# Optimization experiments

Measured on AMD Instinct MI355X. Metric: run time of the kernel, lower is better.

## Reference

```python
import jax, jax.numpy as jnp
import numpy as np

N_USERS, N_ITEMS, D, L = 100000, 30000, 64, 2
N = N_USERS + N_ITEMS
NNZ_ADJ, NNZ_SYM, NNZ_HERB = 4000000, 1600000, 480000


def spmm(rows, cols, vals, x, n):
    # sparse [n, m] @ dense [m, d] via gather + segment_sum
    return jax.ops.segment_sum(vals[:, None] * x[cols], rows, num_segments=n)


def setup_inputs():
    key = jax.random.key(0)
    ks = jax.random.split(key, 19)
    s = np.float32(1.0 / np.sqrt(D))  # xavier-like scale, keeps tanh unsaturated
    return {
        'user_embedding': jax.random.normal(ks[0], (N_USERS, D), jnp.float32) * s,
        'item_embedding': jax.random.normal(ks[1], (N_ITEMS, D), jnp.float32) * s,
        'adj_vals': jax.random.uniform(ks[2], (NNZ_ADJ,), jnp.float32),
        'sym_vals': jax.random.uniform(ks[3], (NNZ_SYM,), jnp.float32),
        'herb_vals': jax.random.uniform(ks[4], (NNZ_HERB,), jnp.float32),
        'Q_user': jax.random.normal(ks[5], (L, D, D), jnp.float32) * s,
        'Q_item': jax.random.normal(ks[6], (L, D, D), jnp.float32) * s,
        'W_gc_user': jax.random.normal(ks[7], (L, 2 * D, D), jnp.float32) * s,
        'W_gc_item': jax.random.normal(ks[8], (L, 2 * D, D), jnp.float32) * s,
        'b_gc_user': jax.random.normal(ks[9], (L, D), jnp.float32) * s,
        'b_gc_item': jax.random.normal(ks[10], (L, D), jnp.float32) * s,
        'M_user': jax.random.normal(ks[11], (D, D), jnp.float32) * s,
        'M_item': jax.random.normal(ks[12], (D, D), jnp.float32) * s,
        'adj_rows': jax.random.randint(ks[13], (NNZ_ADJ,), 0, N, jnp.int32),
        'adj_cols': jax.random.randint(ks[14], (NNZ_ADJ,), 0, N, jnp.int32),
        'sym_rows': jax.random.randint(ks[15], (NNZ_SYM,), 0, N_USERS, jnp.int32),
        'sym_cols': jax.random.randint(ks[16], (NNZ_SYM,), 0, N_USERS, jnp.int32),
        'herb_rows': jax.random.randint(ks[17], (NNZ_HERB,), 0, N_ITEMS, jnp.int32),
        'herb_cols': jax.random.randint(ks[18], (NNZ_HERB,), 0, N_ITEMS, jnp.int32),
    }


def reference(user_embedding, item_embedding, adj_vals, sym_vals, herb_vals,
              Q_user, Q_item, W_gc_user, W_gc_item, b_gc_user, b_gc_item,
              M_user, M_item, adj_rows, adj_cols, sym_rows, sym_cols,
              herb_rows, herb_cols):
    ego0 = jnp.concatenate([user_embedding, item_embedding], axis=0)  # [N, D]

    def graphsage_branch(Q, W, b):
        ego = ego0
        for k in range(L):  # loop over fixed small n_layers
            agg = spmm(adj_rows, adj_cols, adj_vals, ego, N)           # neighbor aggregate
            h = jnp.tanh(agg @ Q[k])                                    # Q transform
            ego = jnp.tanh(jnp.concatenate([ego, h], axis=1) @ W[k] + b[k])
            # mess_dropout = 0 -> identity (eval mode)
        nrm = jnp.sqrt(jnp.sum(ego * ego, axis=1, keepdims=True))
        return ego / jnp.maximum(nrm, 1e-12)                            # F.normalize(p=2, dim=1)

    u_all = graphsage_branch(Q_user, W_gc_user, b_gc_user)
    i_all = graphsage_branch(Q_item, W_gc_item, b_gc_item)
    u_g = u_all[:N_USERS]
    i_g = i_all[N_USERS:]

    user_pair = jnp.tanh(spmm(sym_rows, sym_cols, sym_vals, user_embedding, N_USERS) @ M_user)
    item_pair = jnp.tanh(spmm(herb_rows, herb_cols, herb_vals, item_embedding, N_ITEMS) @ M_item)

    # fusion == 'add'
    return jnp.concatenate([u_g + user_pair, i_g + item_pair], axis=0)  # [N, D]
```

## Files before the change

kernel.cpp:

```cpp
#include <hip/hip_runtime.h>
#include <hip/hip_fp16.h>

#define NU 100000
#define NI 30000
#define NT 130000
#define D  64
#define NNZ_ADJ  4000000
#define NNZ_SYM  1600000
#define NNZ_HERB 480000

#define CHUNK 4096
#define BROWS 512

#define NBLK_ADJ  977
#define NBLK_SYM  391
#define NBLK_HERB 118

#define NBUCK_ADJ  254
#define NBUCK_SYM  196
#define NBUCK_HERB 59
#define CAP_ADJ  17000
#define CAP_SYM  9500
#define CAP_HERB 9500

#define OFF_QU0 0
#define OFF_QI0 4096
#define OFF_QU1 8192
#define OFF_QI1 12288
#define OFF_WU0 16384
#define OFF_WI0 24576
#define OFF_WU1 32768
#define OFF_WI1 40960
#define OFF_MU  49152
#define OFF_MI  53248
#define WT_ELEMS 57344

typedef _Float16 f16x8 __attribute__((ext_vector_type(8)));
typedef float f32x4 __attribute__((ext_vector_type(4)));

__device__ inline f32x4 mfma_16x16x32(f16x8 a, f16x8 b, f32x4 c) {
  return __builtin_amdgcn_mfma_f32_16x16x32_f16(a, b, c, 0, 0, 0);
}
__device__ inline f16x8 ld8h(const __half* p) { return *(const f16x8*)p; }

__device__ inline float pk_val(unsigned p) {
  return __half2float(__ushort_as_half((unsigned short)(p & 0x7fffu)));
}

__global__ __launch_bounds__(256) void binA_all(
    const int* __restrict__ r0, const int* __restrict__ c0,
    const float* __restrict__ v0, uint2* __restrict__ st0, int* __restrict__ bc0,
    const int* __restrict__ r1, const int* __restrict__ c1,
    const float* __restrict__ v1, uint2* __restrict__ st1, int* __restrict__ bc1,
    const int* __restrict__ r2, const int* __restrict__ c2,
    const float* __restrict__ v2, uint2* __restrict__ st2, int* __restrict__ bc2) {
  __shared__ int cnt[256], lexc[256], cur[256], gbase[256], wt[4];
  __shared__ uint2 lpk[CHUNK];
  __shared__ unsigned char bid[CHUNK];
  int blk = blockIdx.x;
  const int* rows; const int* cols; const float* vals;
  uint2* staging; int* bcnt; int nnz, cap, base;
  if (blk < NBLK_ADJ) {
    rows = r0; cols = c0; vals = v0; staging = st0; bcnt = bc0;
    nnz = NNZ_ADJ; cap = CAP_ADJ; base = blk * CHUNK;
  } else if (blk < NBLK_ADJ + NBLK_SYM) {
    rows = r1; cols = c1; vals = v1; staging = st1; bcnt = bc1;
    nnz = NNZ_SYM; cap = CAP_SYM; base = (blk - NBLK_ADJ) * CHUNK;
  } else {
    rows = r2; cols = c2; vals = v2; staging = st2; bcnt = bc2;
    nnz = NNZ_HERB; cap = CAP_HERB; base = (blk - NBLK_ADJ - NBLK_SYM) * CHUNK;
  }
  int tid = threadIdx.x;
  int lim = min(CHUNK, nnz - base);
  cnt[tid] = 0;
  __syncthreads();
  for (int j = tid; j < lim; j += 256) {
    int r = rows[base + j];
    atomicAdd(&cnt[r >> 9], 1);
  }
  __syncthreads();
  int lane = tid & 63, w = tid >> 6;
  int v = cnt[tid];
  int s = v;
#pragma unroll
  for (int o = 1; o < 64; o <<= 1) {
    int t = __shfl_up(s, o, 64);
    if (lane >= o) s += t;
  }
  if (lane == 63) wt[w] = s;
  __syncthreads();
  int woff = 0;
  for (int j = 0; j < w; ++j) woff += wt[j];
  int exc = woff + s - v;
  lexc[tid] = exc;
  cur[tid] = exc;
  gbase[tid] = (v > 0) ? atomicAdd(&bcnt[tid], v) : 0;
  __syncthreads();
  for (int j = tid; j < lim; j += 256) {
    int r = rows[base + j];
    int b = r >> 9;
    unsigned short hv = __half_as_ushort(__float2half(vals[base + j])) & 0x7fffu;
    unsigned cv = ((unsigned)cols[base + j] << 15) | hv;
    int pos = atomicAdd(&cur[b], 1);
    lpk[pos] = make_uint2((unsigned)r, cv);
    bid[pos] = (unsigned char)b;
  }
  __syncthreads();
  for (int i = tid; i < lim; i += 256) {
    int b = bid[i];
    int d = gbase[b] + (i - lexc[b]);
    if (d < cap) staging[(size_t)b * cap + d] = lpk[i];
  }
}

__global__ __launch_bounds__(256) void bucket_scan3(
    int* __restrict__ bc, int* __restrict__ bb,
    int* __restrict__ ptr0, int* __restrict__ ptr1, int* __restrict__ ptr2) {
  __shared__ int wt[4];
  int g = blockIdx.x;
  const int* bcnt = bc + g * 256;
  int* bbase = bb + g * 256;
  int nbuck = g == 0 ? NBUCK_ADJ : g == 1 ? NBUCK_SYM : NBUCK_HERB;
  int n = g == 0 ? NT : g == 1 ? NU : NI;
  int* ptr = g == 0 ? ptr0 : g == 1 ? ptr1 : ptr2;
  int tid = threadIdx.x, lane = tid & 63, w = tid >> 6;
  int v = (tid < nbuck) ? bcnt[tid] : 0;
  int s = v;
#pragma unroll
  for (int o = 1; o < 64; o <<= 1) {
    int t = __shfl_up(s, o, 64);
    if (lane >= o) s += t;
  }
  if (lane == 63) wt[w] = s;
  __syncthreads();
  int woff = 0;
  for (int j = 0; j < w; ++j) woff += wt[j];
  if (tid < nbuck) bbase[tid] = woff + s - v;
  if (tid == 0) ptr[n] = wt[0] + wt[1] + wt[2] + wt[3];
}

__global__ __launch_bounds__(256) void binB_all(
    const uint2* __restrict__ st0, const int* __restrict__ bc0,
    const int* __restrict__ bb0, unsigned* __restrict__ pk0, int* __restrict__ ptr0,
    const uint2* __restrict__ st1, const int* __restrict__ bc1,
    const int* __restrict__ bb1, unsigned* __restrict__ pk1, int* __restrict__ ptr1,
    const uint2* __restrict__ st2, const int* __restrict__ bc2,
    const int* __restrict__ bb2, unsigned* __restrict__ pk2, int* __restrict__ ptr2) {
  __shared__ int rof[512];
  __shared__ int wt[4];
  int blk = blockIdx.x, tid = threadIdx.x;
  const uint2* staging; const int* bcnt; const int* bbase;
  unsigned* pk; int* ptr; int n, cap, b;
  if (blk < NBUCK_ADJ) {
    staging = st0; bcnt = bc0; bbase = bb0; pk = pk0; ptr = ptr0;
    n = NT; cap = CAP_ADJ; b = blk;
  } else if (blk < NBUCK_ADJ + NBUCK_SYM) {
    staging = st1; bcnt = bc1; bbase = bb1; pk = pk1; ptr = ptr1;
    n = NU; cap = CAP_SYM; b = blk - NBUCK_ADJ;
  } else {
    staging = st2; bcnt = bc2; bbase = bb2; pk = pk2; ptr = ptr2;
    n = NI; cap = CAP_HERB; b = blk - NBUCK_ADJ - NBUCK_SYM;
  }
  int cntb = min(bcnt[b], cap);
  int gb = bbase[b];
  const uint2* st = staging + (size_t)b * cap;
  for (int i = tid; i < 512; i += 256) rof[i] = 0;
  __syncthreads();
  for (int i = tid; i < cntb; i += 256) atomicAdd(&rof[st[i].x & 511], 1);
  __syncthreads();
  int v0 = rof[2 * tid], v1 = rof[2 * tid + 1], pv = v0 + v1;
  int lane = tid & 63, w = tid >> 6, s = pv;
#pragma unroll
  for (int o = 1; o < 64; o <<= 1) {
    int t = __shfl_up(s, o, 64);
    if (lane >= o) s += t;
  }
  if (lane == 63) wt[w] = s;
  __syncthreads();
  int woff = 0;
  for (int j = 0; j < w; ++j) woff += wt[j];
  int exc = woff + s - pv;
  int r0 = b * BROWS + 2 * tid;
  if (r0 < n) ptr[r0] = gb + exc;
  if (r0 + 1 < n) ptr[r0 + 1] = gb + exc + v0;
  rof[2 * tid] = exc;
  rof[2 * tid + 1] = exc + v0;
  __syncthreads();
  for (int i = tid; i < cntb; i += 256) {
    uint2 e = st[i];
    int pos = atomicAdd(&rof[e.x & 511], 1);
    pk[gb + pos] = e.y;
  }
}

__global__ __launch_bounds__(256) void to_half(
    const float* __restrict__ U, const float* __restrict__ I,
    __half* __restrict__ EH) {
  int idx = blockIdx.x * 256 + threadIdx.x;
  const int ub = NU * D / 4;
  float4 v = idx < ub ? ((const float4*)U)[idx] : ((const float4*)I)[idx - ub];
  __half2* dst = (__half2*)EH + (size_t)idx * 2;
  dst[0] = __floats2half2_rn(v.x, v.y);
  dst[1] = __floats2half2_rn(v.z, v.w);
}

__global__ __launch_bounds__(256) void prep_weights(
    const float* __restrict__ Qu, const float* __restrict__ Qi,
    const float* __restrict__ Wu, const float* __restrict__ Wi,
    const float* __restrict__ Mu, const float* __restrict__ Mi,
    __half* __restrict__ WT) {
  int gid = blockIdx.x * 256 + threadIdx.x;
  if (gid >= WT_ELEMS) return;
  const float* src;
  int e, K, base;
  if (gid < 16384) {
    int m = gid >> 12; e = gid & 4095; K = 64; base = m * 4096;
    src = (m == 0) ? Qu : (m == 1) ? Qi : (m == 2) ? Qu + 4096 : Qi + 4096;
  } else if (gid < 49152) {
    int t = gid - 16384;
    int m = t >> 13; e = t & 8191; K = 128; base = 16384 + m * 8192;
    src = (m == 0) ? Wu : (m == 1) ? Wi : (m == 2) ? Wu + 8192 : Wi + 8192;
  } else {
    int t = gid - 49152;
    int m = t >> 12; e = t & 4095; K = 64; base = 49152 + m * 4096;
    src = (m == 0) ? Mu : Mi;
  }
  int k = e >> 6, c = e & 63;
  WT[base + c * K + k] = __float2half(src[(size_t)k * 64 + c]);
}

#define EDGE(p)                                        \
  {                                                    \
    __half2 x = Xb[(size_t)((p) >> 15) * XSTRIDE];     \
    float vv = pk_val(p);                              \
    ax += vv * __half2float(__low2half(x));            \
    ay += vv * __half2float(__high2half(x));           \
  }

#define SPMM_BODY()                                    \
  float ax = 0.f, ay = 0.f;                            \
  int i = s;                                           \
  for (; i + 7 < e; i += 8) {                          \
    unsigned q0 = pk[i], q1 = pk[i + 1], q2 = pk[i + 2], q3 = pk[i + 3]; \
    unsigned q4 = pk[i + 4], q5 = pk[i + 5], q6 = pk[i + 6], q7 = pk[i + 7]; \
    EDGE(q0) EDGE(q1) EDGE(q2) EDGE(q3)                \
    EDGE(q4) EDGE(q5) EDGE(q6) EDGE(q7)                \
  }                                                    \
  for (; i + 3 < e; i += 4) {                          \
    unsigned q0 = pk[i], q1 = pk[i + 1], q2 = pk[i + 2], q3 = pk[i + 3]; \
    EDGE(q0) EDGE(q1) EDGE(q2) EDGE(q3)                \
  }                                                    \
  for (; i < e; ++i) { unsigned q = pk[i]; EDGE(q) }

__global__ __launch_bounds__(256) void spmm2_agg0(
    const int* __restrict__ ptr, const unsigned* __restrict__ pk,
    const __half* __restrict__ EH, __half* __restrict__ AGG0h) {
  int wid = (blockIdx.x * 256 + threadIdx.x) >> 5;
  int lane = threadIdx.x & 31;
  if (wid >= NT) return;
  const __half2* Xb = (const __half2*)EH + lane;
  int s = ptr[wid], e = ptr[wid + 1];
#define XSTRIDE 32
  SPMM_BODY()
#undef XSTRIDE
  ((__half2*)AGG0h)[(size_t)wid * 32 + lane] = __floats2half2_rn(ax, ay);
}

__global__ __launch_bounds__(256) void spmm2_agg1(
    const int* __restrict__ ptr, const unsigned* __restrict__ pk,
    const __half* __restrict__ ECH, __half* __restrict__ AGGh) {
  int wid = (blockIdx.x * 256 + threadIdx.x) >> 5;
  int lane = threadIdx.x & 31;
  if (wid >= NT) return;
  const __half2* Xb = (const __half2*)(ECH + (wid < NU ? 0 : 64)) + lane;
  int s = ptr[wid], e = ptr[wid + 1];
#define XSTRIDE 64
  SPMM_BODY()
#undef XSTRIDE
  ((__half2*)AGGh)[(size_t)wid * 32 + lane] = __floats2half2_rn(ax, ay);
}

__global__ __launch_bounds__(256) void spmm2_pair(
    const int* __restrict__ ptr, const unsigned* __restrict__ pk,
    const __half* __restrict__ X, __half* __restrict__ Y, int n) {
  int wid = (blockIdx.x * 256 + threadIdx.x) >> 5;
  int lane = threadIdx.x & 31;
  if (wid >= n) return;
  const __half2* Xb = (const __half2*)X + lane;
  int s = ptr[wid], e = ptr[wid + 1];
#define XSTRIDE 32
  SPMM_BODY()
#undef XSTRIDE
  ((__half2*)Y)[(size_t)wid * 32 + lane] = __floats2half2_rn(ax, ay);
}

__global__ __launch_bounds__(256) void l0_mfma(
    const __half* __restrict__ AGG0h, const __half* __restrict__ EH,
    __half* __restrict__ ECH, const __half* __restrict__ WT,
    const float* __restrict__ bu, const float* __restrict__ bi) {
  __shared__ __half Hs[2][16][72];
  int tid = threadIdx.x;
  int wave = tid >> 6, lane = tid & 63;
  int rl = lane & 15, kg = lane >> 4;
  int rb = blockIdx.x * 16;
  int colg = wave * 16 + rl;

  const __half* Xr = AGG0h + (size_t)(rb + rl) * D + kg * 8;
  f16x8 ax0 = ld8h(Xr), ax1 = ld8h(Xr + 32);
  const __half* qu = WT + OFF_QU0 + (size_t)colg * 64 + kg * 8;
  const __half* qi = WT + OFF_QI0 + (size_t)colg * 64 + kg * 8;
  f32x4 hu = {0.f, 0.f, 0.f, 0.f}, hi = {0.f, 0.f, 0.f, 0.f};
  hu = mfma_16x16x32(ax0, ld8h(qu), hu);
  hu = mfma_16x16x32(ax1, ld8h(qu + 32), hu);
  hi = mfma_16x16x32(ax0, ld8h(qi), hi);
  hi = mfma_16x16x32(ax1, ld8h(qi + 32), hi);
#pragma unroll
  for (int r = 0; r < 4; ++r) {
    int row = kg * 4 + r;
    Hs[0][row][colg] = __float2half(tanhf(hu[r]));
    Hs[1][row][colg] = __float2half(tanhf(hi[r]));
  }
  __syncthreads();

  const __half* Er = EH + (size_t)(rb + rl) * D + kg * 8;
  f16x8 ae0 = ld8h(Er), ae1 = ld8h(Er + 32);
  f16x8 au0 = *(const f16x8*)&Hs[0][rl][kg * 8];
  f16x8 au1 = *(const f16x8*)&Hs[0][rl][32 + kg * 8];
  f16x8 ai0 = *(const f16x8*)&Hs[1][rl][kg * 8];
  f16x8 ai1 = *(const f16x8*)&Hs[1][rl][32 + kg * 8];
  const __half* wu = WT + OFF_WU0 + (size_t)colg * 128 + kg * 8;
  const __half* wi = WT + OFF_WI0 + (size_t)colg * 128 + kg * 8;
  f32x4 su = {0.f, 0.f, 0.f, 0.f}, si = {0.f, 0.f, 0.f, 0.f};
  su = mfma_16x16x32(ae0, ld8h(wu), su);
  su = mfma_16x16x32(ae1, ld8h(wu + 32), su);
  su = mfma_16x16x32(au0, ld8h(wu + 64), su);
  su = mfma_16x16x32(au1, ld8h(wu + 96), su);
  si = mfma_16x16x32(ae0, ld8h(wi), si);
  si = mfma_16x16x32(ae1, ld8h(wi + 32), si);
  si = mfma_16x16x32(ai0, ld8h(wi + 64), si);
  si = mfma_16x16x32(ai1, ld8h(wi + 96), si);
  float bbu = bu[colg], bbi = bi[colg];
#pragma unroll
  for (int r = 0; r < 4; ++r) {
    size_t row = (size_t)(rb + kg * 4 + r);
    ECH[row * 128 + colg] = __float2half(tanhf(su[r] + bbu));
    ECH[row * 128 + 64 + colg] = __float2half(tanhf(si[r] + bbi));
  }
}

__global__ __launch_bounds__(256) void l1_mfma(
    const __half* __restrict__ AGGh, const __half* __restrict__ ECH,
    const __half* __restrict__ PAIR, const __half* __restrict__ WT,
    int qoff, int woff, int moff,
    const float* __restrict__ b1, float* __restrict__ out,
    int row_start, int ec_off) {
  __shared__ __half Hs[16][72];
  __shared__ float Ss[16][68], Ps[16][68];
  int tid = threadIdx.x;
  int wave = tid >> 6, lane = tid & 63;
  int rl = lane & 15, kg = lane >> 4;
  int rb = row_start + blockIdx.x * 16;
  int colg = wave * 16 + rl;

  const __half* Xr = AGGh + (size_t)(rb + rl) * D + kg * 8;
  f16x8 ax0 = ld8h(Xr), ax1 = ld8h(Xr + 32);
  const __half* q1 = WT + qoff + (size_t)colg * 64 + kg * 8;
  f32x4 h = {0.f, 0.f, 0.f, 0.f};
  h = mfma_16x16x32(ax0, ld8h(q1), h);
  h = mfma_16x16x32(ax1, ld8h(q1 + 32), h);
#pragma unroll
  for (int r = 0; r < 4; ++r) Hs[kg * 4 + r][colg] = __float2half(tanhf(h[r]));
  __syncthreads();

  const __half* Er = ECH + (size_t)(rb + rl) * 128 + ec_off + kg * 8;
  f16x8 ae0 = ld8h(Er), ae1 = ld8h(Er + 32);
  f16x8 ah0 = *(const f16x8*)&Hs[rl][kg * 8];
  f16x8 ah1 = *(const f16x8*)&Hs[rl][32 + kg * 8];
  const __half* Pr = PAIR + (size_t)(rb + rl) * D + kg * 8;
  f16x8 ap0 = ld8h(Pr), ap1 = ld8h(Pr + 32);
  const __half* w1 = WT + woff + (size_t)colg * 128 + kg * 8;
  const __half* mm = WT + moff + (size_t)colg * 64 + kg * 8;
  f32x4 s = {0.f, 0.f, 0.f, 0.f}, sp = {0.f, 0.f, 0.f, 0.f};
  s = mfma_16x16x32(ae0, ld8h(w1), s);
  s = mfma_16x16x32(ae1, ld8h(w1 + 32), s);
  s = mfma_16x16x32(ah0, ld8h(w1 + 64), s);
  s = mfma_16x16x32(ah1, ld8h(w1 + 96), s);
  sp = mfma_16x16x32(ap0, ld8h(mm), sp);
  sp = mfma_16x16x32(ap1, ld8h(mm + 32), sp);
  float bb = b1[colg];
#pragma unroll
  for (int r = 0; r < 4; ++r) {
    Ss[kg * 4 + r][colg] = tanhf(s[r] + bb);
    Ps[kg * 4 + r][colg] = tanhf(sp[r]);
  }
  __syncthreads();

  int lr = tid >> 4, q = tid & 15;
  float4 v = *(float4*)&Ss[lr][q * 4];
  float4 p = *(float4*)&Ps[lr][q * 4];
  float ss = v.x * v.x + v.y * v.y + v.z * v.z + v.w * v.w;
  ss += __shfl_xor(ss, 1, 16);
  ss += __shfl_xor(ss, 2, 16);
  ss += __shfl_xor(ss, 4, 16);
  ss += __shfl_xor(ss, 8, 16);
  float inv = 1.0f / fmaxf(sqrtf(ss), 1e-12f);
  *(float4*)&out[(size_t)(rb + lr) * D + q * 4] =
      make_float4(v.x * inv + p.x, v.y * inv + p.y,
                  v.z * inv + p.z, v.w * inv + p.w);
}

extern "C" void kernel_launch(void* const* d_in, const int* in_sizes, int n_in,
                              void* d_out, int out_size, void* d_ws, size_t ws_size,
                              hipStream_t stream) {
  const float* user_emb = (const float*)d_in[0];
  const float* item_emb = (const float*)d_in[1];
  const float* adj_vals = (const float*)d_in[2];
  const float* sym_vals = (const float*)d_in[3];
  const float* herb_vals = (const float*)d_in[4];
  const float* Q_user = (const float*)d_in[5];
  const float* Q_item = (const float*)d_in[6];
  const float* W_user = (const float*)d_in[7];
  const float* W_item = (const float*)d_in[8];
  const float* b_user = (const float*)d_in[9];
  const float* b_item = (const float*)d_in[10];
  const float* M_user = (const float*)d_in[11];
  const float* M_item = (const float*)d_in[12];
  const int* adj_rows = (const int*)d_in[13];
  const int* adj_cols = (const int*)d_in[14];
  const int* sym_rows = (const int*)d_in[15];
  const int* sym_cols = (const int*)d_in[16];
  const int* herb_rows = (const int*)d_in[17];
  const int* herb_cols = (const int*)d_in[18];

  float* out = (float*)d_out;

  char* w = (char*)d_ws;
  size_t off = 0;
  auto alloc = [&](size_t bytes) -> void* {
    off = (off + 255) & ~(size_t)255;
    void* p = w + off;
    off += bytes;
    return p;
  };
  __half* EH    = (__half*)alloc((size_t)NT * D * 2);
  __half* AGG0h = (__half*)alloc((size_t)NT * D * 2);
  __half* ECH   = (__half*)alloc((size_t)NT * 128 * 2);
  __half* AGGh  = (__half*)alloc((size_t)NT * D * 2);
  int* ptr_adj  = (int*)alloc((size_t)(NT + 1) * 4);
  unsigned* pk_adj = (unsigned*)alloc((size_t)NNZ_ADJ * 4);
  int* ptr_sym  = (int*)alloc((size_t)(NU + 1) * 4);
  unsigned* pk_sym = (unsigned*)alloc((size_t)NNZ_SYM * 4);
  int* ptr_herb = (int*)alloc((size_t)(NI + 1) * 4);
  unsigned* pk_herb = (unsigned*)alloc((size_t)NNZ_HERB * 4);
  int* bc = (int*)alloc(768 * 4);
  int* bb = (int*)alloc(768 * 4);
  __half* WT = (__half*)alloc((size_t)WT_ELEMS * 2);

  uint2* st_adj  = (uint2*)ECH;
  uint2* st_sym  = (uint2*)AGG0h;
  uint2* st_herb = (uint2*)EH;

  prep_weights<<<(WT_ELEMS + 255) / 256, 256, 0, stream>>>(
      Q_user, Q_item, W_user, W_item, M_user, M_item, WT);

  hipMemsetAsync(bc, 0, 768 * 4, stream);
  binA_all<<<NBLK_ADJ + NBLK_SYM + NBLK_HERB, 256, 0, stream>>>(
      adj_rows, adj_cols, adj_vals, st_adj, bc,
      sym_rows, sym_cols, sym_vals, st_sym, bc + 256,
      herb_rows, herb_cols, herb_vals, st_herb, bc + 512);
  bucket_scan3<<<3, 256, 0, stream>>>(bc, bb, ptr_adj, ptr_sym, ptr_herb);
  binB_all<<<NBUCK_ADJ + NBUCK_SYM + NBUCK_HERB, 256, 0, stream>>>(
      st_adj, bc, bb, pk_adj, ptr_adj,
      st_sym, bc + 256, bb + 256, pk_sym, ptr_sym,
      st_herb, bc + 512, bb + 512, pk_herb, ptr_herb);

  to_half<<<NT * D / 4 / 256, 256, 0, stream>>>(user_emb, item_emb, EH);

  spmm2_agg0<<<NT / 8, 256, 0, stream>>>(ptr_adj, pk_adj, EH, AGG0h);
  l0_mfma<<<NT / 16, 256, 0, stream>>>(AGG0h, EH, ECH, WT, b_user, b_item);

  spmm2_pair<<<NU / 8, 256, 0, stream>>>(ptr_sym, pk_sym, EH, AGG0h, NU);
  spmm2_pair<<<NI / 8, 256, 0, stream>>>(
      ptr_herb, pk_herb, EH + (size_t)NU * D, AGG0h + (size_t)NU * D, NI);

  spmm2_agg1<<<NT / 8, 256, 0, stream>>>(ptr_adj, pk_adj, ECH, AGGh);

  l1_mfma<<<NU / 16, 256, 0, stream>>>(
      AGGh, ECH, AGG0h, WT, OFF_QU1, OFF_WU1, OFF_MU, b_user + 64, out, 0, 0);
  l1_mfma<<<NI / 16, 256, 0, stream>>>(
      AGGh, ECH, AGG0h, WT, OFF_QI1, OFF_WI1, OFF_MI, b_item + 64, out, NU, 64);
}
```

Before: 433.2 us.

## Fuse pair and layer-1 SpMM launches into one kernel; halve binning chunk

Merges the two pairwise SpMM launches and the layer-1 adjacency SpMM into a single kernel that chooses its CSR source per warp by row range. This removes two launch boundaries and lets the lighter pair rows fill in alongside the adj rows. The binning kernel's chunk size is halved, doubling its block count, and the per-entry bucket-id shared array is dropped in favour of recomputing the bucket from the stored row. The gather stride becomes a runtime shift in the fused kernel, which adds a little per-warp branching.

```diff
diff --git a/kernel.cpp b/kernel.cpp
--- a/kernel.cpp
+++ b/kernel.cpp
@@ -9,12 +9,12 @@
 #define NNZ_SYM  1600000
 #define NNZ_HERB 480000
 
-#define CHUNK 4096
+#define CHUNK 2048
 #define BROWS 512
 
-#define NBLK_ADJ  977
-#define NBLK_SYM  391
-#define NBLK_HERB 118
+#define NBLK_ADJ  1954
+#define NBLK_SYM  782
+#define NBLK_HERB 235
 
 #define NBUCK_ADJ  254
 #define NBUCK_SYM  196
@@ -56,7 +56,6 @@
     const float* __restrict__ v2, uint2* __restrict__ st2, int* __restrict__ bc2) {
   __shared__ int cnt[256], lexc[256], cur[256], gbase[256], wt[4];
   __shared__ uint2 lpk[CHUNK];
-  __shared__ unsigned char bid[CHUNK];
   int blk = blockIdx.x;
   const int* rows; const int* cols; const float* vals;
   uint2* staging; int* bcnt; int nnz, cap, base;
@@ -103,13 +102,13 @@
     unsigned cv = ((unsigned)cols[base + j] << 15) | hv;
     int pos = atomicAdd(&cur[b], 1);
     lpk[pos] = make_uint2((unsigned)r, cv);
-    bid[pos] = (unsigned char)b;
   }
   __syncthreads();
   for (int i = tid; i < lim; i += 256) {
-    int b = bid[i];
+    uint2 e = lpk[i];
+    int b = (int)(e.x >> 9);
     int d = gbase[b] + (i - lexc[b]);
-    if (d < cap) staging[(size_t)b * cap + d] = lpk[i];
+    if (d < cap) staging[(size_t)b * cap + d] = e;
   }
 }
 
@@ -231,7 +230,7 @@
 
 #define EDGE(p)                                        \
   {                                                    \
-    __half2 x = Xb[(size_t)((p) >> 15) * XSTRIDE];     \
+    __half2 x = Xb[(size_t)((p) >> 15) << XSHIFT];     \
     float vv = pk_val(p);                              \
     ax += vv * __half2float(__low2half(x));            \
     ay += vv * __half2float(__high2half(x));           \
@@ -260,38 +259,42 @@
   if (wid >= NT) return;
   const __half2* Xb = (const __half2*)EH + lane;
   int s = ptr[wid], e = ptr[wid + 1];
-#define XSTRIDE 32
+#define XSHIFT 5
   SPMM_BODY()
-#undef XSTRIDE
+#undef XSHIFT
   ((__half2*)AGG0h)[(size_t)wid * 32 + lane] = __floats2half2_rn(ax, ay);
 }
 
-__global__ __launch_bounds__(256) void spmm2_agg1(
-    const int* __restrict__ ptr, const unsigned* __restrict__ pk,
-    const __half* __restrict__ ECH, __half* __restrict__ AGGh) {
+#define NROWS_FUSED (NT + NU + NI)
+__global__ __launch_bounds__(256) void spmm2_fused(
+    const int* __restrict__ ptr_adj, const unsigned* __restrict__ pk_adj,
+    const int* __restrict__ ptr_sym, const unsigned* __restrict__ pk_sym,
+    const int* __restrict__ ptr_herb, const unsigned* __restrict__ pk_herb,
+    const __half* __restrict__ ECH, const __half* __restrict__ EH,
+    __half* __restrict__ AGGh, __half* __restrict__ PAIR) {
   int wid = (blockIdx.x * 256 + threadIdx.x) >> 5;
   int lane = threadIdx.x & 31;
-  if (wid >= NT) return;
-  const __half2* Xb = (const __half2*)(ECH + (wid < NU ? 0 : 64)) + lane;
-  int s = ptr[wid], e = ptr[wid + 1];
-#define XSTRIDE 64
+  if (wid >= NROWS_FUSED) return;
+  const int* ptrg; const unsigned* pk; const __half2* Xb; __half2* Yp;
+  int xshift, r;
+  if (wid < NT) {
+    r = wid; ptrg = ptr_adj; pk = pk_adj; xshift = 6;
+    Xb = (const __half2*)(ECH + (r < NU ? 0 : 64)) + lane;
+    Yp = (__half2*)AGGh + (size_t)r * 32 + lane;
+  } else if (wid < NT + NU) {
+    r = wid - NT; ptrg = ptr_sym; pk = pk_sym; xshift = 5;
+    Xb = (const __half2*)EH + lane;
+    Yp = (__half2*)PAIR + (size_t)r * 32 + lane;
+  } else {
+    r = wid - NT - NU; ptrg = ptr_herb; pk = pk_herb; xshift = 5;
+    Xb = (const __half2*)(EH + (size_t)NU * D) + lane;
+    Yp = (__half2*)(PAIR + (size_t)NU * D) + (size_t)r * 32 + lane;
+  }
+  int s = ptrg[r], e = ptrg[r + 1];
+#define XSHIFT xshift
   SPMM_BODY()
-#undef XSTRIDE
-  ((__half2*)AGGh)[(size_t)wid * 32 + lane] = __floats2half2_rn(ax, ay);
-}
-
-__global__ __launch_bounds__(256) void spmm2_pair(
-    const int* __restrict__ ptr, const unsigned* __restrict__ pk,
-    const __half* __restrict__ X, __half* __restrict__ Y, int n) {
-  int wid = (blockIdx.x * 256 + threadIdx.x) >> 5;
-  int lane = threadIdx.x & 31;
-  if (wid >= n) return;
-  const __half2* Xb = (const __half2*)X + lane;
-  int s = ptr[wid], e = ptr[wid + 1];
-#define XSTRIDE 32
-  SPMM_BODY()
-#undef XSTRIDE
-  ((__half2*)Y)[(size_t)wid * 32 + lane] = __floats2half2_rn(ax, ay);
+#undef XSHIFT
+  *Yp = __floats2half2_rn(ax, ay);
 }
 
 __global__ __launch_bounds__(256) void l0_mfma(
@@ -479,11 +482,9 @@
   spmm2_agg0<<<NT / 8, 256, 0, stream>>>(ptr_adj, pk_adj, EH, AGG0h);
   l0_mfma<<<NT / 16, 256, 0, stream>>>(AGG0h, EH, ECH, WT, b_user, b_item);
 
-  spmm2_pair<<<NU / 8, 256, 0, stream>>>(ptr_sym, pk_sym, EH, AGG0h, NU);
-  spmm2_pair<<<NI / 8, 256, 0, stream>>>(
-      ptr_herb, pk_herb, EH + (size_t)NU * D, AGG0h + (size_t)NU * D, NI);
-
-  spmm2_agg1<<<NT / 8, 256, 0, stream>>>(ptr_adj, pk_adj, ECH, AGGh);
+  spmm2_fused<<<NROWS_FUSED / 8, 256, 0, stream>>>(
+      ptr_adj, pk_adj, ptr_sym, pk_sym, ptr_herb, pk_herb,
+      ECH, EH, AGGh, AGG0h);
 
   l1_mfma<<<NU / 16, 256, 0, stream>>>(
       AGGh, ECH, AGG0h, WT, OFF_QU1, OFF_WU1, OFF_MU, b_user + 64, out, 0, 0);
```

Measured after the change: 445.1 us. 1.03x slower.
